# Performance work log

Hardware: AMD Instinct MI355X
Metric: run time of the kernel (lower is better)

Reference implementation:

```python
import jax, jax.numpy as jnp
import numpy as np

A, D, TOTAL = 1024, 128, 524288


def setup_inputs() -> dict:
    key = jax.random.key(0)
    k1, k2, k3 = jax.random.split(key, 3)
    anchors = jax.random.normal(k1, (A, D), dtype=jnp.float32)
    Xn_flat = jax.random.normal(k2, (TOTAL, D), dtype=jnp.float32)
    segment_ids = jnp.sort(jax.random.randint(k3, (TOTAL,), 0, A))
    return {"anchors": anchors, "Xn_flat": Xn_flat, "segment_ids": segment_ids}


def reference(anchors, Xn_flat, segment_ids):
    # anchors: [A, D]; Xn_flat: [TOTAL, D] (ragged segments flattened);
    # segment_ids: [TOTAL] row -> anchor index (sorted).
    d_feat = anchors.shape[1]
    eps = 1e-4 / d_feat  # eps = 0.0001 / x1.size(0), x1 = anchor vector of size D
    # L2dist(p=2, squared=False): sqrt(sum(|x1-x2|^2, dim=1) + eps)
    diff = jnp.abs(Xn_flat - anchors[segment_ids])          # [TOTAL, D]
    sq_dist = jnp.sum(diff * diff, axis=1)                  # [TOTAL]
    dist = jnp.sqrt(sq_dist + eps)                          # [TOTAL]
    # per-anchor sum of distances, then log1p, accumulated over anchors
    per_anchor = jax.ops.segment_sum(dist, segment_ids, num_segments=anchors.shape[0])  # [A]
    intra_class_dist = jnp.sum(jnp.log1p(per_anchor))
    n_total = Xn_flat.shape[0]  # N = sum of segment lengths
    return intra_class_dist / n_total
```

## Files before the change

kernel.cpp:

```cpp
#include <hip/hip_runtime.h>
#include <math.h>

#define DFEAT 128

__global__ __launch_bounds__(256) void seg_bounds_kernel(
    const int* __restrict__ seg, int* __restrict__ offs, int total, int A)
{
    const int i = blockIdx.x * 256 + threadIdx.x;
    if (i >= total) return;
    const int s = seg[i];
    const int p = (i == 0) ? -1 : seg[i - 1];
    for (int a = p + 1; a <= s; ++a) offs[a] = i;
    if (i == total - 1)
        for (int a = s + 1; a <= A; ++a) offs[a] = total;
}

__global__ __launch_bounds__(256) void icc_anchor_kernel(
    const float* __restrict__ anchors,
    const float* __restrict__ Xn,
    const int*   __restrict__ offs,
    float*       __restrict__ out,
    float inv_total)
{
    const int a    = blockIdx.x;
    const int tid  = threadIdx.x;
    const int lane = tid & 31;
    const int hw   = tid >> 5;
    const float eps = 1e-4f / (float)DFEAT;

    const int lo = offs[a];
    const int hi = offs[a + 1];

    const float4 av = *reinterpret_cast<const float4*>(
        anchors + (size_t)a * DFEAT + lane * 4);

    float dsum = 0.0f;
    for (int row = lo + hw; row < hi; row += 8) {
        const float4 x = *reinterpret_cast<const float4*>(
            Xn + (size_t)row * DFEAT + lane * 4);
        const float dx = x.x - av.x;
        const float dy = x.y - av.y;
        const float dz = x.z - av.z;
        const float dw = x.w - av.w;
        float sq = dx * dx + dy * dy + dz * dz + dw * dw;
        #pragma unroll
        for (int off = 16; off > 0; off >>= 1)
            sq += __shfl_down(sq, off, 32);
        if (lane == 0) dsum += sqrtf(sq + eps);
    }

    __shared__ float part[8];
    if (lane == 0) part[hw] = dsum;
    __syncthreads();
    if (tid == 0) {
        float s = 0.0f;
        #pragma unroll
        for (int h = 0; h < 8; ++h) s += part[h];
        atomicAdd(out, log1pf(s) * inv_total);
    }
}

extern "C" void kernel_launch(void* const* d_in, const int* in_sizes, int n_in,
                              void* d_out, int out_size, void* d_ws, size_t ws_size,
                              hipStream_t stream) {
    const float* anchors = (const float*)d_in[0];
    const float* Xn      = (const float*)d_in[1];
    const int*   seg     = (const int*)d_in[2];
    float* out = (float*)d_out;

    const int A     = in_sizes[0] / DFEAT;
    const int total = in_sizes[2];

    int* offs = (int*)d_ws;

    hipMemsetAsync(out, 0, sizeof(float), stream);
    seg_bounds_kernel<<<(total + 255) / 256, 256, 0, stream>>>(seg, offs, total, A);
    icc_anchor_kernel<<<A, 256, 0, stream>>>(anchors, Xn, offs, out,
                                             1.0f / (float)total);
}
```

Baseline: 377.2 us.

## Fuse segment bounds via binary search and use 4-lane row reductions

Drops the separate segment-bounds kernel: each block now finds its own anchor's row range by binary searching the sorted segment ids. Each row is handled by 4 lanes, each loading 8 float4 chunks, so only two short shuffles are needed per row instead of a 5-step 32-lane shuffle. The block size grows to 512 and partial sums are combined with a 64-wide wavefront reduction. This saves a kernel launch and shuffle overhead and adds more loads in flight per thread, at the cost of less contiguous access within each load instruction.

```diff
diff --git a/kernel.cpp b/kernel.cpp
--- a/kernel.cpp
+++ b/kernel.cpp
@@ -2,60 +2,71 @@
 #include <math.h>
 
 #define DFEAT 128
+#define BLOCK 512
 
-__global__ __launch_bounds__(256) void seg_bounds_kernel(
-    const int* __restrict__ seg, int* __restrict__ offs, int total, int A)
-{
-    const int i = blockIdx.x * 256 + threadIdx.x;
-    if (i >= total) return;
-    const int s = seg[i];
-    const int p = (i == 0) ? -1 : seg[i - 1];
-    for (int a = p + 1; a <= s; ++a) offs[a] = i;
-    if (i == total - 1)
-        for (int a = s + 1; a <= A; ++a) offs[a] = total;
-}
-
-__global__ __launch_bounds__(256) void icc_anchor_kernel(
+__global__ __launch_bounds__(BLOCK) void icc_anchor_kernel(
     const float* __restrict__ anchors,
     const float* __restrict__ Xn,
-    const int*   __restrict__ offs,
+    const int*   __restrict__ seg,
     float*       __restrict__ out,
-    float inv_total)
+    int total, float inv_total)
 {
-    const int a    = blockIdx.x;
-    const int tid  = threadIdx.x;
-    const int lane = tid & 31;
-    const int hw   = tid >> 5;
+    const int a   = blockIdx.x;
+    const int tid = threadIdx.x;
+    __shared__ int   bnd[2];
+    __shared__ float part[BLOCK / 64];
+
+    if (tid >= BLOCK - 2) {
+        const int key = a + (tid & 1);
+        int lo = 0, hi = total;
+        while (lo < hi) {
+            const int m = (lo + hi) >> 1;
+            if (seg[m] < key) lo = m + 1; else hi = m;
+        }
+        bnd[tid & 1] = lo;
+    }
+
+    const int l4 = tid & 3;
+    const int q  = (tid & 63) >> 2;
+    const int w  = tid >> 6;
     const float eps = 1e-4f / (float)DFEAT;
 
-    const int lo = offs[a];
-    const int hi = offs[a + 1];
+    float4 afrag[8];
+    #pragma unroll
+    for (int k = 0; k < 8; ++k)
+        afrag[k] = *reinterpret_cast<const float4*>(
+            anchors + (size_t)a * DFEAT + k * 16 + l4 * 4);
 
-    const float4 av = *reinterpret_cast<const float4*>(
-        anchors + (size_t)a * DFEAT + lane * 4);
+    __syncthreads();
+    const int lo = bnd[0], hi = bnd[1];
 
     float dsum = 0.0f;
-    for (int row = lo + hw; row < hi; row += 8) {
-        const float4 x = *reinterpret_cast<const float4*>(
-            Xn + (size_t)row * DFEAT + lane * 4);
-        const float dx = x.x - av.x;
-        const float dy = x.y - av.y;
-        const float dz = x.z - av.z;
-        const float dw = x.w - av.w;
-        float sq = dx * dx + dy * dy + dz * dz + dw * dw;
+    for (int row = lo + w * 16 + q; row < hi; row += BLOCK / 4) {
+        const float* rp = Xn + (size_t)row * DFEAT + l4 * 4;
+        float sq = 0.0f;
         #pragma unroll
-        for (int off = 16; off > 0; off >>= 1)
-            sq += __shfl_down(sq, off, 32);
-        if (lane == 0) dsum += sqrtf(sq + eps);
+        for (int k = 0; k < 8; ++k) {
+            const float4 x = *reinterpret_cast<const float4*>(rp + k * 16);
+            const float dx = x.x - afrag[k].x;
+            const float dy = x.y - afrag[k].y;
+            const float dz = x.z - afrag[k].z;
+            const float dw = x.w - afrag[k].w;
+            sq += dx * dx + dy * dy + dz * dz + dw * dw;
+        }
+        sq += __shfl_xor(sq, 1, 4);
+        sq += __shfl_xor(sq, 2, 4);
+        if (l4 == 0) dsum += sqrtf(sq + eps);
     }
 
-    __shared__ float part[8];
-    if (lane == 0) part[hw] = dsum;
+    #pragma unroll
+    for (int off = 32; off > 0; off >>= 1)
+        dsum += __shfl_down(dsum, off, 64);
+    if ((tid & 63) == 0) part[w] = dsum;
     __syncthreads();
     if (tid == 0) {
         float s = 0.0f;
         #pragma unroll
-        for (int h = 0; h < 8; ++h) s += part[h];
+        for (int h = 0; h < BLOCK / 64; ++h) s += part[h];
         atomicAdd(out, log1pf(s) * inv_total);
     }
 }
@@ -71,10 +82,7 @@
     const int A     = in_sizes[0] / DFEAT;
     const int total = in_sizes[2];
 
-    int* offs = (int*)d_ws;
-
     hipMemsetAsync(out, 0, sizeof(float), stream);
-    seg_bounds_kernel<<<(total + 255) / 256, 256, 0, stream>>>(seg, offs, total, A);
-    icc_anchor_kernel<<<A, 256, 0, stream>>>(anchors, Xn, offs, out,
-                                             1.0f / (float)total);
+    icc_anchor_kernel<<<A, BLOCK, 0, stream>>>(anchors, Xn, seg, out,
+                                               total, 1.0f / (float)total);
 }
```

Measured after the change: 374.5 us. About the same (-0.7%).
